# Performance work log

Measured on AMD Instinct MI355X. Metric: run time of the kernel, lower is better.

## Reference

```python
import jax, jax.numpy as jnp
import numpy as np

# Irreps config: node = 64x0e + 32x1o, edge sh = 1x0e + 1x1o
N, E = 50000, 800000
MUL0, MUL1 = 64, 32
D_IN = MUL0 + 3 * MUL1          # 160
FC_H = 64
W_NUMEL = MUL0 + MUL0 + MUL1 + MUL1  # 192, per-instruction uvu weights
SQRT3 = 1.7320508075688772
ACT_C = 1.6791   # e3nn normalize2mom constant for silu


def setup_inputs() -> dict:
    key = jax.random.key(0)
    ks = jax.random.split(key, 11)
    return {
        "x": jax.random.normal(ks[0], (N, D_IN), jnp.float32),
        "edge_scalars": jax.random.uniform(ks[1], (E, FC_H), dtype=jnp.float32),
        "edge_attr_sh": jax.random.normal(ks[2], (E, 4), jnp.float32),
        "edge_index": jax.random.randint(ks[3], (2, E), 0, N),
        "w_fc1": jax.random.normal(ks[4], (FC_H, FC_H), jnp.float32),
        "w_fc2": jax.random.normal(ks[5], (FC_H, W_NUMEL), jnp.float32),
        "w_sc_s": jax.random.normal(ks[6], (MUL0, MUL0), jnp.float32),
        "w_sc_v": jax.random.normal(ks[7], (MUL1, MUL1), jnp.float32),
        "w_lin_s": jax.random.normal(ks[8], (96, MUL0), jnp.float32),
        "w_lin_v": jax.random.normal(ks[9], (96, MUL1), jnp.float32),
        "w_alpha": jax.random.normal(ks[10], (96, 1), jnp.float32) * 0.1,
    }


def reference(x, edge_scalars, edge_attr_sh, edge_index, w_fc1, w_fc2,
              w_sc_s, w_sc_v, w_lin_s, w_lin_v, w_alpha):
    src, dst = edge_index[0], edge_index[1]

    # --- fc: FullyConnectedNet([64, 64, 192], silu), e3nn fan-in norm ---
    h = jax.nn.silu(edge_scalars @ w_fc1 / np.sqrt(FC_H)) * ACT_C
    weight = h @ w_fc2 / np.sqrt(FC_H)                       # [E, 192]
    w0 = weight[:, :MUL0]                 # 0e x 0e -> 0e (mul 64)
    w1 = weight[:, MUL0:2 * MUL0]         # 0e x 1o -> 1o (mul 64)
    w2 = weight[:, 2 * MUL0:2 * MUL0 + MUL1]   # 1o x 0e -> 1o (mul 32)
    w3 = weight[:, 2 * MUL0 + MUL1:]           # 1o x 1o -> 0e (mul 32)

    # --- self connection: o3.Linear(in -> out), per-irrep mixing ---
    x_s = x[:, :MUL0]                                   # [N, 64]
    x_v = x[:, MUL0:].reshape(N, MUL1, 3)               # [N, 32, 3]
    sc_s = x_s @ w_sc_s / np.sqrt(MUL0)
    sc_v = jnp.einsum('nui,uw->nwi', x_v, w_sc_v) / np.sqrt(MUL1)
    sc_out = jnp.concatenate([sc_s, sc_v.reshape(N, 3 * MUL1)], axis=1)

    # --- gather + edge-weighted uvu tensor product ---
    gx_s = x_s[src]                                     # [E, 64]
    gx_v = x_v[src]                                     # [E, 32, 3]
    sh_s = edge_attr_sh[:, 0:1]                         # [E, 1]
    sh_v = edge_attr_sh[:, 1:4]                         # [E, 3]

    # path weights fold with w3j so factors cancel for 1o outputs
    mid_s0 = w0 * gx_s * sh_s                                        # [E,64] 0e
    mid_s1 = w3 * jnp.einsum('eui,ei->eu', gx_v, sh_v) / SQRT3       # [E,32] 0e
    mid_v0 = w1[:, :, None] * gx_s[:, :, None] * sh_v[:, None, :]    # [E,64,3] 1o
    mid_v1 = w2[:, :, None] * gx_v * sh_s[:, :, None]                # [E,32,3] 1o
    edge_feat = jnp.concatenate(
        [mid_s0, mid_s1, mid_v0.reshape(E, 3 * MUL0), mid_v1.reshape(E, 3 * MUL1)],
        axis=1)                                                      # [E, 384]

    # --- scatter-mean to destination nodes ---
    seg = jax.ops.segment_sum(edge_feat, dst, num_segments=N)
    cnt = jax.ops.segment_sum(jnp.ones((E,), edge_feat.dtype), dst, num_segments=N)
    mean = seg / jnp.maximum(cnt, 1.0)[:, None]                      # [N, 384]

    m_s = mean[:, :96]                                   # 96x0e
    m_v = mean[:, 96:].reshape(N, 96, 3)                 # 96x1o

    # --- alpha gate (o3.Linear mid -> 0e) and output linear ---
    alpha = m_s @ w_alpha / np.sqrt(96)                  # [N, 1]
    lin_s = m_s @ w_lin_s / np.sqrt(96)                  # [N, 64]
    lin_v = jnp.einsum('nui,uw->nwi', m_v, w_lin_v) / np.sqrt(96)
    lin_out = jnp.concatenate([lin_s, lin_v.reshape(N, 3 * MUL1)], axis=1)

    # sc.output_mask is all-ones here (every output irrep reachable)
    return sc_out + alpha * lin_out
```

## Files before the change

kernel.cpp:

```cpp
#include <hip/hip_runtime.h>
#include <hip/hip_bf16.h>

#define N_NODES 50000
#define N_EDGES 800000
#define MUL0 64
#define MUL1 32
#define D_IN 160
#define FC_H 64
#define W_NUMEL 192
#define FEAT 384
#define ACT_C 1.6791f
#define INV_SQRT3 0.57735026918962576f
#define RSQRT32 0.17677669529663687f
#define RSQRT96 0.10206207261596575f

#define TILE 64
#define NWG_EDGE (N_EDGES / TILE)

typedef __attribute__((ext_vector_type(8))) short s16x8;
typedef __attribute__((ext_vector_type(4))) float f32x4;
typedef _Float16 h8 __attribute__((ext_vector_type(8)));
typedef __fp16 fp16x2 __attribute__((ext_vector_type(2)));

static __device__ __forceinline__ unsigned short f2bf(float f) {
    __hip_bfloat16 b = __float2bfloat16(f);
    return __builtin_bit_cast(unsigned short, b);
}

static __device__ __forceinline__ int swz(int row, int byte_in_row) {
    int unit = ((row & 1) << 2) | (byte_in_row >> 4);
    int su = unit ^ ((row >> 1) & 7);
    return (row >> 1) * 128 + su * 16 + (byte_in_row & 15);
}
static __device__ __forceinline__ h8 rdh8(const unsigned char* base, int row, int eb) {
    return *(const h8*)(base + swz(row, eb));
}


#define HIST_NB ((N_EDGES + 255) / 256)
#define XCONV_NB ((N_NODES * D_IN + 4095) / 4096)

__global__ __launch_bounds__(256) void hist_prep_kernel(
    const int*   __restrict__ eidx,
    int*         __restrict__ cnt,
    const float* __restrict__ w_fc1,
    const float* __restrict__ w_fc2,
    const float* __restrict__ w_sc_s,
    const float* __restrict__ w_sc_v,
    const float* __restrict__ w_lin_s,
    const float* __restrict__ w_lin_v,
    const float* __restrict__ x,
    unsigned short* __restrict__ x16,
    unsigned short* __restrict__ w1t,
    unsigned short* __restrict__ w2t,
    unsigned short* __restrict__ wscs_t,
    unsigned short* __restrict__ wscv_t,
    unsigned short* __restrict__ wlins_t,
    unsigned short* __restrict__ wlinv_t)
{
    int b = blockIdx.x;
    if (b < HIST_NB) {
        int e = b * 256 + threadIdx.x;
        if (e < N_EDGES) atomicAdd(&cnt[eidx[N_EDGES + e]], 1);
    } else if (b < HIST_NB + 48) {
        int i = (b - HIST_NB) * 256 + threadIdx.x;
        if (i < 64 * 64)  w1t[i]    = f2bf(w_fc1[(i & 63) * FC_H + (i >> 6)]);
        if (i < 192 * 64) w2t[i]    = f2bf(w_fc2[(i & 63) * W_NUMEL + (i >> 6)]);
        if (i < 64 * 64)  wscs_t[i] = f2bf(w_sc_s[(i & 63) * 64 + (i >> 6)]);
        if (i < 32 * 32)  wscv_t[i] = f2bf(w_sc_v[(i & 31) * 32 + (i >> 5)]);
        if (i < 64 * 96)  wlins_t[i] = f2bf(w_lin_s[(i % 96) * 64 + (i / 96)]);
        if (i < 32 * 96)  wlinv_t[i] = f2bf(w_lin_v[(i % 96) * 32 + (i / 96)]);
    } else {
        size_t i0 = ((size_t)(b - HIST_NB - 48) * 256 + threadIdx.x) * 16;
        if (i0 < (size_t)N_NODES * D_IN) {
            const float4* src = (const float4*)(x + i0);
            unsigned short u[16];
#pragma unroll
            for (int k = 0; k < 4; ++k) {
                float4 v = src[k];
                u[k * 4 + 0] = __builtin_bit_cast(unsigned short, (_Float16)v.x);
                u[k * 4 + 1] = __builtin_bit_cast(unsigned short, (_Float16)v.y);
                u[k * 4 + 2] = __builtin_bit_cast(unsigned short, (_Float16)v.z);
                u[k * 4 + 3] = __builtin_bit_cast(unsigned short, (_Float16)v.w);
            }
            uint4* dst = (uint4*)(x16 + i0);
            dst[0] = *(const uint4*)&u[0];
            dst[1] = *(const uint4*)&u[8];
        }
    }
}

#define SCAN_NB 64
#define SCAN_CH ((N_NODES + SCAN_NB - 1) / SCAN_NB)

__global__ __launch_bounds__(256) void scanA_kernel(const int* __restrict__ cnt,
                                                    int* __restrict__ bsum) {
    __shared__ int sred[4];
    int b = blockIdx.x, t = threadIdx.x;
    int lim = min((b + 1) * SCAN_CH, N_NODES);
    int s = 0;
    for (int i = b * SCAN_CH + t; i < lim; i += 256) s += cnt[i];
    for (int d = 1; d < 64; d <<= 1) s += __shfl_xor(s, d);
    if ((t & 63) == 0) sred[t >> 6] = s;
    __syncthreads();
    if (t == 0) bsum[b] = sred[0] + sred[1] + sred[2] + sred[3];
}

__global__ __launch_bounds__(256) void scanC_kernel(const int* __restrict__ cnt,
                                                    const int* __restrict__ bsum,
                                                    int* __restrict__ fill) {
    __shared__ int s_w[4];
    __shared__ int s_boff;
    int b = blockIdx.x, t = threadIdx.x;
    if (t < 64) {
        int v = bsum[t];
        int p = v;
        for (int d = 1; d < 64; d <<= 1) { int u = __shfl_up(p, d); if (t >= d) p += u; }
        if (t == b) s_boff = p - v;
    }
    const int CH2 = (SCAN_CH + 255) / 256;
    int base = b * SCAN_CH + t * CH2;
    int lim = min((b + 1) * SCAN_CH, N_NODES);
    int s = 0;
#pragma unroll
    for (int k = 0; k < CH2; ++k) { int i = base + k; if (i < lim) s += cnt[i]; }
    int v = s;
    for (int d = 1; d < 64; d <<= 1) { int u = __shfl_up(v, d); if ((t & 63) >= d) v += u; }
    if ((t & 63) == 63) s_w[t >> 6] = v;
    __syncthreads();
    if (t == 0) { int run = 0; for (int w = 0; w < 4; ++w) { int tv = s_w[w]; s_w[w] = run; run += tv; } }
    __syncthreads();
    int run = s_boff + s_w[t >> 6] + (v - s);
#pragma unroll
    for (int k = 0; k < CH2; ++k) {
        int i = base + k;
        if (i < lim) { fill[i] = run; run += cnt[i]; }
    }
}

__global__ __launch_bounds__(256) void scatter_ids_kernel(const int* __restrict__ eidx,
                                                          int* __restrict__ fill,
                                                          int* __restrict__ sorted_eid,
                                                          int* __restrict__ sorted_src,
                                                          int* __restrict__ sorted_dst) {
    int e = blockIdx.x * 256 + threadIdx.x;
    if (e < N_EDGES) {
        int d = eidx[N_EDGES + e];
        int s = eidx[e];
        int p = atomicAdd(&fill[d], 1);
        sorted_eid[p] = e;
        sorted_src[p] = s;
        sorted_dst[p] = d;
    }
}

#define X_OFF    0
#define W_OFF    20480
#define SH_OFF   45056
#define SID_OFF  45568
#define SEGN_OFF 45696
#define NSEG_OFF 45952
#define SMEM_SZ  45968

static __device__ __forceinline__ h8 seg_mask(const unsigned* vv, unsigned tgt) {
    h8 a;
#pragma unroll
    for (int w2 = 0; w2 < 4; ++w2) {
        a[w2 * 2]     = ((vv[w2] & 0xffffu) == tgt) ? (_Float16)1.f : (_Float16)0.f;
        a[w2 * 2 + 1] = ((vv[w2] >> 16)     == tgt) ? (_Float16)1.f : (_Float16)0.f;
    }
    return a;
}

__global__ __launch_bounds__(256) void edge_kernel(
    const unsigned short* __restrict__ x16,
    const float* __restrict__ es,
    const float* __restrict__ sh,
    const int*   __restrict__ sorted_eid,
    const int*   __restrict__ sorted_src,
    const int*   __restrict__ sorted_dst,
    const unsigned short* __restrict__ w1t,
    const unsigned short* __restrict__ w2t,
    float* __restrict__ accg)
{
    __shared__ __align__(16) unsigned char smem[SMEM_SZ];
    int* s_segnode = (int*)(smem + SEGN_OFF);
    unsigned short* s_sid = (unsigned short*)(smem + SID_OFF);

    const int t = threadIdx.x;
    const int l = t & 63;
    const int wv = t >> 6;
    const int lr = l & 15;
    const int lk = l >> 4;
    int bid;
    {
        const int nwg = NWG_EDGE;
        int orig = blockIdx.x;
        int xcd = orig & 7, idx = orig >> 3;
        int q = nwg >> 3, r = nwg & 7;
        bid = (xcd < r ? xcd * (q + 1) : r * (q + 1) + (xcd - r) * q) + idx;
    }
    const int tile0 = bid * TILE;

    int eid_own = sorted_eid[tile0 + wv * 16 + lr];
    float4 esf[4];
    {
        const float4* ep = (const float4*)(es + (size_t)eid_own * FC_H);
        esf[0] = ep[lk * 2];     esf[1] = ep[lk * 2 + 1];
        esf[2] = ep[8 + lk * 2]; esf[3] = ep[8 + lk * 2 + 1];
    }
    const int hs   = t >> 7;
    const int tt_h = t & 127;
    const int xe   = tt_h & 31;
    const int cgrp = tt_h >> 5;
    float4 xg[5];
    {
        const float4* xp = (const float4*)(x16 + (size_t)sorted_src[tile0 + hs * 32 + xe] * D_IN);
#pragma unroll
        for (int k = 0; k < 5; ++k) xg[k] = xp[cgrp * 5 + k];
    }
    float shv = sh[(size_t)sorted_eid[tile0 + (t >> 2)] * 4 + (t & 3)];
    if (wv == 0) {
        int dl = sorted_dst[tile0 + l];
        int nd = __shfl_down(dl, 1);
        bool flag = (l == 63) || (dl != nd);
        unsigned long long m = __ballot(flag);
        int sid = __popcll(m & ((1ull << l) - 1ull));
        s_sid[l] = (unsigned short)sid;
        if (flag) s_segnode[sid] = dl;
        if (l == 63) *(int*)(smem + NSEG_OFF) = sid + 1;
    }

    unsigned short* s_h = (unsigned short*)(smem + X_OFF);
    s16x8 afrag[2];
    {
        s16x8 a;
        a[0] = f2bf(esf[0].x); a[1] = f2bf(esf[0].y); a[2] = f2bf(esf[0].z); a[3] = f2bf(esf[0].w);
        a[4] = f2bf(esf[1].x); a[5] = f2bf(esf[1].y); a[6] = f2bf(esf[1].z); a[7] = f2bf(esf[1].w);
        afrag[0] = a;
        a[0] = f2bf(esf[2].x); a[1] = f2bf(esf[2].y); a[2] = f2bf(esf[2].z); a[3] = f2bf(esf[2].w);
        a[4] = f2bf(esf[3].x); a[5] = f2bf(esf[3].y); a[6] = f2bf(esf[3].z); a[7] = f2bf(esf[3].w);
        afrag[1] = a;
    }
#pragma unroll
    for (int nt = 0; nt < 4; ++nt) {
        f32x4 hacc = {0.f, 0.f, 0.f, 0.f};
#pragma unroll
        for (int kk = 0; kk < 2; ++kk) {
            s16x8 b = *(const s16x8*)(w1t + (nt * 16 + lr) * 64 + kk * 32 + lk * 8);
            hacc = __builtin_amdgcn_mfma_f32_16x16x32_bf16(afrag[kk], b, hacc, 0, 0, 0);
        }
#pragma unroll
        for (int q = 0; q < 4; ++q) {
            float aa = hacc[q] * 0.125f;
            float hv = aa * (1.f / (1.f + __expf(-aa))) * ACT_C;
            s_h[(wv * 16 + lk * 4 + q) * 72 + nt * 16 + lr] = f2bf(hv);
        }
    }
    s16x8 hfrag[2];
#pragma unroll
    for (int kk = 0; kk < 2; ++kk)
        hfrag[kk] = *(const s16x8*)(s_h + (wv * 16 + lr) * 72 + kk * 32 + lk * 8);
    __syncthreads();

    {
        const int ws = wv >> 1;
        const int ebyte = (wv & 1) * 32 + lk * 8;
        unsigned char* bw = smem + W_OFF + ws * 12288;
#pragma unroll
        for (int nt = 0; nt < 12; ++nt) {
            f32x4 acc = {0.f, 0.f, 0.f, 0.f};
#pragma unroll
            for (int kk = 0; kk < 2; ++kk) {
                s16x8 b = *(const s16x8*)(w2t + (nt * 16 + lr) * 64 + kk * 32 + lk * 8);
                acc = __builtin_amdgcn_mfma_f32_16x16x32_bf16(hfrag[kk], b, acc, 0, 0, 0);
            }
            int f = nt * 16 + lr;
            fp16x2 p0 = __builtin_amdgcn_cvt_pkrtz(acc[0] * 0.125f, acc[1] * 0.125f);
            fp16x2 p1 = __builtin_amdgcn_cvt_pkrtz(acc[2] * 0.125f, acc[3] * 0.125f);
            uint2 wval = { __builtin_bit_cast(unsigned, p0), __builtin_bit_cast(unsigned, p1) };
            *(uint2*)(bw + swz(f, ebyte)) = wval;
        }
    }
    {
        unsigned char* bx = smem + X_OFF + hs * 10240;
#pragma unroll
        for (int k = 0; k < 5; ++k) {
            unsigned short u[8];
            *(float4*)u = xg[k];
#pragma unroll
            for (int jj = 0; jj < 8; ++jj) {
                int r = (cgrp * 5 + k) * 8 + jj;
                *(unsigned short*)(bx + swz(r, xe * 2)) = u[jj];
            }
        }
    }
    {
        int e = t >> 2, c = t & 3;
        *(_Float16*)(smem + SH_OFF + (e >> 5) * 256 + swz(c, (e & 31) * 2)) = (_Float16)shv;
    }
    __syncthreads();

    const int nseg = *(const int*)(smem + NSEG_OFF);
    const int eb = lk * 16;

    h8 shreg[4][2];
    unsigned vv[2][4];
#pragma unroll
    for (int ks = 0; ks < 2; ++ks) {
#pragma unroll
        for (int r = 0; r < 4; ++r)
            shreg[r][ks] = rdh8(smem + SH_OFF + ks * 256, r, eb);
        uint4 sv = *(const uint4*)(smem + SID_OFF + ks * 64 + lk * 16);
        vv[ks][0] = sv.x; vv[ks][1] = sv.y; vv[ks][2] = sv.z; vv[ks][3] = sv.w;
    }

    h8 Bv[4][2];
    int fcol[4];
    bool cls3j[4] = {false, false, false, false};
#pragma unroll
    for (int ks = 0; ks < 2; ++ks) {
        const unsigned char* bx = smem + X_OFF + ks * 10240;
        const unsigned char* bw = smem + W_OFF + ks * 12288;
        if (wv == 0) {
#pragma unroll
            for (int jj = 0; jj < 4; ++jj) {
                int col = jj * 16 + lr;
                Bv[jj][ks] = rdh8(bw, col, eb) * rdh8(bx, col, eb);
                fcol[jj] = col;
            }
        } else if (wv == 1) {
#pragma unroll
            for (int jj = 0; jj < 4; ++jj) {
                int col = jj * 16 + lr;
                Bv[jj][ks] = rdh8(bw, 128 + col / 3, eb) * rdh8(bx, 64 + col, eb);
                fcol[jj] = 288 + col;
            }
        } else if (wv == 2) {
#pragma unroll
            for (int jj = 0; jj < 2; ++jj) {
                int col = 64 + jj * 16 + lr;
                Bv[jj][ks] = rdh8(bw, 128 + col / 3, eb) * rdh8(bx, 64 + col, eb);
                fcol[jj] = 288 + col;
            }
#pragma unroll
            for (int jj = 2; jj < 4; ++jj) {
                int col = (jj - 2) * 16 + lr;
                h8 d = rdh8(bx, 64 + 3 * col, eb)     * shreg[1][ks]
                     + rdh8(bx, 64 + 3 * col + 1, eb) * shreg[2][ks]
                     + rdh8(bx, 64 + 3 * col + 2, eb) * shreg[3][ks];
                Bv[jj][ks] = rdh8(bw, 160 + col, eb) * d;
                fcol[jj] = 64 + col;
                cls3j[jj] = true;
            }
        } else {
#pragma unroll
            for (int jj = 0; jj < 4; ++jj) {
                int col = jj * 16 + lr;
                Bv[jj][ks] = rdh8(bw, 64 + col, eb) * rdh8(bx, col, eb);
                fcol[jj] = 96 + 3 * col;
            }
        }
    }

    if (wv != 3) {
        const int npass = (nseg + 15) >> 4;
        for (int p = 0; p < npass; ++p) {
            h8 bm0 = seg_mask(vv[0], (unsigned)(p * 16 + lr));
            h8 bm1 = seg_mask(vv[1], (unsigned)(p * 16 + lr));
            h8 As0 = bm0 * shreg[0][0];
            h8 As1 = bm1 * shreg[0][1];
            const int m0 = p * 16 + lk * 4;
            float* nptr[4]; bool valid[4], atq[4];
#pragma unroll
            for (int q = 0; q < 4; ++q) {
                int sg = m0 + q;
                valid[q] = sg < nseg;
                int node = valid[q] ? s_segnode[sg] : 0;
                nptr[q] = accg + (size_t)node * FEAT;
                atq[q] = (sg == 0) || (sg == nseg - 1);
            }
#pragma unroll
            for (int jj = 0; jj < 4; ++jj) {
                f32x4 acc = {0.f, 0.f, 0.f, 0.f};
                acc = __builtin_amdgcn_mfma_f32_16x16x32_f16(cls3j[jj] ? bm0 : As0, Bv[jj][0], acc, 0, 0, 0);
                acc = __builtin_amdgcn_mfma_f32_16x16x32_f16(cls3j[jj] ? bm1 : As1, Bv[jj][1], acc, 0, 0, 0);
                const float sc = cls3j[jj] ? INV_SQRT3 : 1.f;
#pragma unroll
                for (int q = 0; q < 4; ++q) {
                    if (valid[q]) {
                        float v = acc[q] * sc;
                        float* a = nptr[q] + fcol[jj];
                        if (atq[q]) atomicAdd(a, v); else *a = v;
                    }
                }
            }
        }
    } else {
        const int npass = (3 * nseg + 15) >> 4;
        for (int p = 0; p < npass; ++p) {
            int m = p * 16 + lr;
            int sgA = m / 3, i3A = m - 3 * sgA;
            h8 mk0 = seg_mask(vv[0], (unsigned)sgA);
            h8 mk1 = seg_mask(vv[1], (unsigned)sgA);
            h8 A0 = mk0 * ((i3A == 0) ? shreg[1][0] : (i3A == 1) ? shreg[2][0] : shreg[3][0]);
            h8 A1 = mk1 * ((i3A == 0) ? shreg[1][1] : (i3A == 1) ? shreg[2][1] : shreg[3][1]);
            int m0 = p * 16 + lk * 4;
            int sgq = m0 / 3, rq = m0 - 3 * sgq;
            float* nptr[4]; int i3q[4]; bool valid[4], atq[4];
#pragma unroll
            for (int q = 0; q < 4; ++q) {
                valid[q] = sgq < nseg;
                int node = valid[q] ? s_segnode[sgq] : 0;
                nptr[q] = accg + (size_t)node * FEAT;
                i3q[q] = rq;
                atq[q] = (sgq == 0) || (sgq == nseg - 1);
                if (++rq == 3) { rq = 0; ++sgq; }
            }
#pragma unroll
            for (int jj = 0; jj < 4; ++jj) {
                f32x4 acc = {0.f, 0.f, 0.f, 0.f};
                acc = __builtin_amdgcn_mfma_f32_16x16x32_f16(A0, Bv[jj][0], acc, 0, 0, 0);
                acc = __builtin_amdgcn_mfma_f32_16x16x32_f16(A1, Bv[jj][1], acc, 0, 0, 0);
#pragma unroll
                for (int q = 0; q < 4; ++q) {
                    if (valid[q]) {
                        float* a = nptr[q] + fcol[jj] + i3q[q];
                        if (atq[q]) atomicAdd(a, acc[q]); else *a = acc[q];
                    }
                }
            }
        }
    }
}


static __device__ __forceinline__ s16x8 frag_c8(const float* p, float s) {
    float4 u = *(const float4*)p, v = *(const float4*)(p + 4);
    s16x8 a;
    a[0] = f2bf(u.x * s); a[1] = f2bf(u.y * s); a[2] = f2bf(u.z * s); a[3] = f2bf(u.w * s);
    a[4] = f2bf(v.x * s); a[5] = f2bf(v.y * s); a[6] = f2bf(v.z * s); a[7] = f2bf(v.w * s);
    return a;
}

__global__ __launch_bounds__(256) void node_kernel(
    const float* __restrict__ x,
    const float* __restrict__ accg,
    const int*   __restrict__ cnt,
    const unsigned short* __restrict__ wscs_t,
    const unsigned short* __restrict__ wscv_t,
    const unsigned short* __restrict__ wlins_t,
    const unsigned short* __restrict__ wlinv_t,
    const float* __restrict__ w_alpha,
    float* __restrict__ out)
{
    const int t = threadIdx.x;
    const int wv = t >> 6, l = t & 63;
    const int lr = l & 15, lk = l >> 4;
    const int n_base = blockIdx.x * 64 + wv * 16;
    const int nrow = n_base + lr;
    const int nclamp = min(nrow, N_NODES - 1);

    const float* mrow = accg + (size_t)nclamp * FEAT;
    const float* xrow = x + (size_t)nclamp * D_IN;
    const float rinv = 1.f / (float)max(cnt[nclamp], 1);

    s16x8 ax[2], ams[3], axv[3], amv[3][3];
#pragma unroll
    for (int kk = 0; kk < 2; ++kk) ax[kk] = frag_c8(xrow + kk * 32 + lk * 8, 1.f);
#pragma unroll
    for (int kk = 0; kk < 3; ++kk) ams[kk] = frag_c8(mrow + kk * 32 + lk * 8, rinv);
    {
        float xb[24];
        const float4* p = (const float4*)(xrow + 64 + 24 * lk);
#pragma unroll
        for (int q = 0; q < 6; ++q) ((float4*)xb)[q] = p[q];
#pragma unroll
        for (int i = 0; i < 3; ++i) {
            s16x8 a;
#pragma unroll
            for (int j = 0; j < 8; ++j) a[j] = f2bf(xb[3 * j + i]);
            axv[i] = a;
        }
    }
#pragma unroll
    for (int kk = 0; kk < 3; ++kk) {
        float mb[24];
        const float4* p = (const float4*)(mrow + 96 + 96 * kk + 24 * lk);
#pragma unroll
        for (int q = 0; q < 6; ++q) ((float4*)mb)[q] = p[q];
#pragma unroll
        for (int i = 0; i < 3; ++i) {
            s16x8 a;
#pragma unroll
            for (int j = 0; j < 8; ++j) a[j] = f2bf(mb[3 * j + i] * rinv);
            amv[i][kk] = a;
        }
    }

    float ap = 0.f;
    {
        float ab[24];
        const float4* p = (const float4*)(mrow + 24 * lk);
#pragma unroll
        for (int q = 0; q < 6; ++q) ((float4*)ab)[q] = p[q];
#pragma unroll
        for (int j = 0; j < 24; ++j) ap += ab[j] * rinv * w_alpha[lk * 24 + j];
    }
    ap += __shfl_xor(ap, 16);
    ap += __shfl_xor(ap, 32);
    const float alphav = ap * RSQRT96;

    f32x4 accA[4], accL[4];
#pragma unroll
    for (int nt = 0; nt < 4; ++nt) { accA[nt] = (f32x4){0,0,0,0}; accL[nt] = (f32x4){0,0,0,0}; }
#pragma unroll
    for (int nt = 0; nt < 4; ++nt) {
#pragma unroll
        for (int kk = 0; kk < 2; ++kk) {
            s16x8 b = *(const s16x8*)(wscs_t + (nt * 16 + lr) * 64 + kk * 32 + lk * 8);
            accA[nt] = __builtin_amdgcn_mfma_f32_16x16x32_bf16(ax[kk], b, accA[nt], 0, 0, 0);
        }
#pragma unroll
        for (int kk = 0; kk < 3; ++kk) {
            s16x8 b = *(const s16x8*)(wlins_t + (nt * 16 + lr) * 96 + kk * 32 + lk * 8);
            accL[nt] = __builtin_amdgcn_mfma_f32_16x16x32_bf16(ams[kk], b, accL[nt], 0, 0, 0);
        }
    }
    f32x4 accVs[3][2], accVl[3][2];
#pragma unroll
    for (int i = 0; i < 3; ++i)
#pragma unroll
        for (int nt = 0; nt < 2; ++nt) { accVs[i][nt] = (f32x4){0,0,0,0}; accVl[i][nt] = (f32x4){0,0,0,0}; }
#pragma unroll
    for (int i = 0; i < 3; ++i) {
#pragma unroll
        for (int nt = 0; nt < 2; ++nt) {
            s16x8 b = *(const s16x8*)(wscv_t + (nt * 16 + lr) * 32 + lk * 8);
            accVs[i][nt] = __builtin_amdgcn_mfma_f32_16x16x32_bf16(axv[i], b, accVs[i][nt], 0, 0, 0);
#pragma unroll
            for (int kk = 0; kk < 3; ++kk) {
                s16x8 b2 = *(const s16x8*)(wlinv_t + (nt * 16 + lr) * 96 + kk * 32 + lk * 8);
                accVl[i][nt] = __builtin_amdgcn_mfma_f32_16x16x32_bf16(amv[i][kk], b2, accVl[i][nt], 0, 0, 0);
            }
        }
    }

#pragma unroll
    for (int q = 0; q < 4; ++q) {
        int row = lk * 4 + q;
        float ar = __shfl(alphav, row);
        int n = n_base + row;
        bool ok = (n < N_NODES);
        float* orow = out + (size_t)n * 160;
#pragma unroll
        for (int nt = 0; nt < 4; ++nt) {
            float vout = accA[nt][q] * 0.125f + ar * accL[nt][q] * RSQRT96;
            if (ok) orow[nt * 16 + lr] = vout;
        }
#pragma unroll
        for (int i = 0; i < 3; ++i)
#pragma unroll
            for (int nt = 0; nt < 2; ++nt) {
                float vout = accVs[i][nt][q] * RSQRT32 + ar * accVl[i][nt][q] * RSQRT96;
                if (ok) orow[64 + 3 * (nt * 16 + lr) + i] = vout;
            }
    }
}


extern "C" void kernel_launch(void* const* d_in, const int* in_sizes, int n_in,
                              void* d_out, int out_size, void* d_ws, size_t ws_size,
                              hipStream_t stream) {
    const float* x        = (const float*)d_in[0];
    const float* es       = (const float*)d_in[1];
    const float* sh       = (const float*)d_in[2];
    const int*   eidx     = (const int*)d_in[3];
    const float* w_fc1    = (const float*)d_in[4];
    const float* w_fc2    = (const float*)d_in[5];
    const float* w_sc_s   = (const float*)d_in[6];
    const float* w_sc_v   = (const float*)d_in[7];
    const float* w_lin_s  = (const float*)d_in[8];
    const float* w_lin_v  = (const float*)d_in[9];
    const float* w_alpha  = (const float*)d_in[10];
    float* out = (float*)d_out;

    float* accg       = (float*)d_ws;
    int*   cnt        = (int*)(accg + (size_t)N_NODES * FEAT);
    int*   fill       = cnt + N_NODES;
    int*   sorted_eid = fill + N_NODES;
    int*   sorted_src = sorted_eid + N_EDGES;
    int*   sorted_dst = sorted_src + N_EDGES;
    unsigned short* w1t     = (unsigned short*)(sorted_dst + N_EDGES);
    unsigned short* w2t     = w1t + 64 * 64;
    unsigned short* wscs_t  = w2t + 192 * 64;
    unsigned short* wscv_t  = wscs_t + 64 * 64;
    unsigned short* wlins_t = wscv_t + 32 * 32;
    unsigned short* wlinv_t = wlins_t + 64 * 96;
    int* bsum = (int*)(wlinv_t + 32 * 96);
    size_t base_bytes = (size_t)((unsigned char*)(bsum + SCAN_NB) - (unsigned char*)d_ws);
    base_bytes = (base_bytes + 15) & ~(size_t)15;
    unsigned short* x16 = (unsigned short*)((unsigned char*)d_ws + base_bytes);

    (void)hipMemsetAsync(d_ws, 0, ((size_t)N_NODES * FEAT + N_NODES) * 4, stream);
    hipLaunchKernelGGL(hist_prep_kernel, dim3(HIST_NB + 48 + XCONV_NB), dim3(256), 0, stream,
                       eidx, cnt, w_fc1, w_fc2, w_sc_s, w_sc_v, w_lin_s, w_lin_v,
                       x, x16, w1t, w2t, wscs_t, wscv_t, wlins_t, wlinv_t);
    hipLaunchKernelGGL(scanA_kernel, dim3(SCAN_NB), dim3(256), 0, stream, cnt, bsum);
    hipLaunchKernelGGL(scanC_kernel, dim3(SCAN_NB), dim3(256), 0, stream, cnt, bsum, fill);
    hipLaunchKernelGGL(scatter_ids_kernel, dim3((N_EDGES + 255) / 256), dim3(256), 0, stream,
                       eidx, fill, sorted_eid, sorted_src, sorted_dst);
    hipLaunchKernelGGL(edge_kernel, dim3(NWG_EDGE), dim3(256), 0, stream,
                       x16, es, sh, sorted_eid, sorted_src, sorted_dst, w1t, w2t, accg);
    hipLaunchKernelGGL(node_kernel, dim3((N_NODES + 63) / 64), dim3(256), 0, stream,
                       x, accg, cnt, wscs_t, wscv_t, wlins_t, wlinv_t, w_alpha, out);
}
```

Measured before the change: 427.8 us.

## Fold accumulator zeroing into prep kernel, merge scans, presort edge SH

```diff
diff --git a/kernel.cpp b/kernel.cpp
--- a/kernel.cpp
+++ b/kernel.cpp
@@ -37,12 +37,14 @@
 }
 
 
-#define HIST_NB ((N_EDGES + 255) / 256)
+#define ZERO_NB  18750
+#define HIST_NB  ((N_EDGES + 255) / 256)
 #define XCONV_NB ((N_NODES * D_IN + 4095) / 4096)
 
 __global__ __launch_bounds__(256) void hist_prep_kernel(
     const int*   __restrict__ eidx,
     int*         __restrict__ cnt,
+    float*       __restrict__ accg,
     const float* __restrict__ w_fc1,
     const float* __restrict__ w_fc2,
     const float* __restrict__ w_sc_s,
@@ -59,11 +61,17 @@
     unsigned short* __restrict__ wlinv_t)
 {
     int b = blockIdx.x;
-    if (b < HIST_NB) {
-        int e = b * 256 + threadIdx.x;
+    if (b < ZERO_NB) {
+        size_t i = ((size_t)b * 256 + threadIdx.x) * 4;
+        if (i < (size_t)N_NODES * FEAT) {
+            float4 z = {0.f, 0.f, 0.f, 0.f};
+            *(float4*)(accg + i) = z;
+        }
+    } else if (b < ZERO_NB + HIST_NB) {
+        int e = (b - ZERO_NB) * 256 + threadIdx.x;
         if (e < N_EDGES) atomicAdd(&cnt[eidx[N_EDGES + e]], 1);
-    } else if (b < HIST_NB + 48) {
-        int i = (b - HIST_NB) * 256 + threadIdx.x;
+    } else if (b < ZERO_NB + HIST_NB + 48) {
+        int i = (b - ZERO_NB - HIST_NB) * 256 + threadIdx.x;
         if (i < 64 * 64)  w1t[i]    = f2bf(w_fc1[(i & 63) * FC_H + (i >> 6)]);
         if (i < 192 * 64) w2t[i]    = f2bf(w_fc2[(i & 63) * W_NUMEL + (i >> 6)]);
         if (i < 64 * 64)  wscs_t[i] = f2bf(w_sc_s[(i & 63) * 64 + (i >> 6)]);
@@ -71,7 +79,7 @@
         if (i < 64 * 96)  wlins_t[i] = f2bf(w_lin_s[(i % 96) * 64 + (i / 96)]);
         if (i < 32 * 96)  wlinv_t[i] = f2bf(w_lin_v[(i % 96) * 32 + (i / 96)]);
     } else {
-        size_t i0 = ((size_t)(b - HIST_NB - 48) * 256 + threadIdx.x) * 16;
+        size_t i0 = ((size_t)(b - ZERO_NB - HIST_NB - 48) * 256 + threadIdx.x) * 16;
         if (i0 < (size_t)N_NODES * D_IN) {
             const float4* src = (const float4*)(x + i0);
             unsigned short u[16];
@@ -93,30 +101,20 @@
 #define SCAN_NB 64
 #define SCAN_CH ((N_NODES + SCAN_NB - 1) / SCAN_NB)
 
-__global__ __launch_bounds__(256) void scanA_kernel(const int* __restrict__ cnt,
-                                                    int* __restrict__ bsum) {
-    __shared__ int sred[4];
-    int b = blockIdx.x, t = threadIdx.x;
-    int lim = min((b + 1) * SCAN_CH, N_NODES);
-    int s = 0;
-    for (int i = b * SCAN_CH + t; i < lim; i += 256) s += cnt[i];
-    for (int d = 1; d < 64; d <<= 1) s += __shfl_xor(s, d);
-    if ((t & 63) == 0) sred[t >> 6] = s;
-    __syncthreads();
-    if (t == 0) bsum[b] = sred[0] + sred[1] + sred[2] + sred[3];
-}
-
-__global__ __launch_bounds__(256) void scanC_kernel(const int* __restrict__ cnt,
-                                                    const int* __restrict__ bsum,
-                                                    int* __restrict__ fill) {
+__global__ __launch_bounds__(256) void scan_kernel(const int* __restrict__ cnt,
+                                                   int* __restrict__ fill) {
     __shared__ int s_w[4];
     __shared__ int s_boff;
     int b = blockIdx.x, t = threadIdx.x;
-    if (t < 64) {
-        int v = bsum[t];
-        int p = v;
-        for (int d = 1; d < 64; d <<= 1) { int u = __shfl_up(p, d); if (t >= d) p += u; }
-        if (t == b) s_boff = p - v;
+    {
+        int lim = min(b * SCAN_CH, N_NODES);
+        int s = 0;
+        for (int i = t; i < lim; i += 256) s += cnt[i];
+        for (int d = 1; d < 64; d <<= 1) s += __shfl_xor(s, d);
+        if ((t & 63) == 0) s_w[t >> 6] = s;
+        __syncthreads();
+        if (t == 0) s_boff = s_w[0] + s_w[1] + s_w[2] + s_w[3];
+        __syncthreads();
     }
     const int CH2 = (SCAN_CH + 255) / 256;
     int base = b * SCAN_CH + t * CH2;
@@ -126,11 +124,13 @@
     for (int k = 0; k < CH2; ++k) { int i = base + k; if (i < lim) s += cnt[i]; }
     int v = s;
     for (int d = 1; d < 64; d <<= 1) { int u = __shfl_up(v, d); if ((t & 63) >= d) v += u; }
+    __syncthreads();
     if ((t & 63) == 63) s_w[t >> 6] = v;
     __syncthreads();
-    if (t == 0) { int run = 0; for (int w = 0; w < 4; ++w) { int tv = s_w[w]; s_w[w] = run; run += tv; } }
-    __syncthreads();
-    int run = s_boff + s_w[t >> 6] + (v - s);
+    int woff = 0;
+#pragma unroll
+    for (int w = 0; w < 4; ++w) if (w < (t >> 6)) woff += s_w[w];
+    int run = s_boff + woff + (v - s);
 #pragma unroll
     for (int k = 0; k < CH2; ++k) {
         int i = base + k;
@@ -139,10 +139,12 @@
 }
 
 __global__ __launch_bounds__(256) void scatter_ids_kernel(const int* __restrict__ eidx,
+                                                          const float* __restrict__ sh,
                                                           int* __restrict__ fill,
                                                           int* __restrict__ sorted_eid,
                                                           int* __restrict__ sorted_src,
-                                                          int* __restrict__ sorted_dst) {
+                                                          int* __restrict__ sorted_dst,
+                                                          float* __restrict__ shs) {
     int e = blockIdx.x * 256 + threadIdx.x;
     if (e < N_EDGES) {
         int d = eidx[N_EDGES + e];
@@ -151,6 +153,7 @@
         sorted_eid[p] = e;
         sorted_src[p] = s;
         sorted_dst[p] = d;
+        *(float4*)(shs + (size_t)p * 4) = *(const float4*)(sh + (size_t)e * 4);
     }
 }
 
@@ -175,7 +178,7 @@
 __global__ __launch_bounds__(256) void edge_kernel(
     const unsigned short* __restrict__ x16,
     const float* __restrict__ es,
-    const float* __restrict__ sh,
+    const float* __restrict__ shs,
     const int*   __restrict__ sorted_eid,
     const int*   __restrict__ sorted_src,
     const int*   __restrict__ sorted_dst,
@@ -219,7 +222,7 @@
 #pragma unroll
         for (int k = 0; k < 5; ++k) xg[k] = xp[cgrp * 5 + k];
     }
-    float shv = sh[(size_t)sorted_eid[tile0 + (t >> 2)] * 4 + (t & 3)];
+    float shv = shs[(size_t)tile0 * 4 + t];
     if (wv == 0) {
         int dl = sorted_dst[tile0 + l];
         int nd = __shfl_down(dl, 1);
@@ -597,21 +600,21 @@
     unsigned short* wscv_t  = wscs_t + 64 * 64;
     unsigned short* wlins_t = wscv_t + 32 * 32;
     unsigned short* wlinv_t = wlins_t + 64 * 96;
-    int* bsum = (int*)(wlinv_t + 32 * 96);
-    size_t base_bytes = (size_t)((unsigned char*)(bsum + SCAN_NB) - (unsigned char*)d_ws);
+    int* pad = (int*)(wlinv_t + 32 * 96);
+    size_t base_bytes = (size_t)((unsigned char*)(pad + SCAN_NB) - (unsigned char*)d_ws);
     base_bytes = (base_bytes + 15) & ~(size_t)15;
     unsigned short* x16 = (unsigned short*)((unsigned char*)d_ws + base_bytes);
-
-    (void)hipMemsetAsync(d_ws, 0, ((size_t)N_NODES * FEAT + N_NODES) * 4, stream);
-    hipLaunchKernelGGL(hist_prep_kernel, dim3(HIST_NB + 48 + XCONV_NB), dim3(256), 0, stream,
-                       eidx, cnt, w_fc1, w_fc2, w_sc_s, w_sc_v, w_lin_s, w_lin_v,
+    float* shs = (float*)(x16 + (size_t)N_NODES * D_IN);
+
+    (void)hipMemsetAsync(cnt, 0, (size_t)N_NODES * 4, stream);
+    hipLaunchKernelGGL(hist_prep_kernel, dim3(ZERO_NB + HIST_NB + 48 + XCONV_NB), dim3(256), 0, stream,
+                       eidx, cnt, accg, w_fc1, w_fc2, w_sc_s, w_sc_v, w_lin_s, w_lin_v,
                        x, x16, w1t, w2t, wscs_t, wscv_t, wlins_t, wlinv_t);
-    hipLaunchKernelGGL(scanA_kernel, dim3(SCAN_NB), dim3(256), 0, stream, cnt, bsum);
-    hipLaunchKernelGGL(scanC_kernel, dim3(SCAN_NB), dim3(256), 0, stream, cnt, bsum, fill);
+    hipLaunchKernelGGL(scan_kernel, dim3(SCAN_NB), dim3(256), 0, stream, cnt, fill);
     hipLaunchKernelGGL(scatter_ids_kernel, dim3((N_EDGES + 255) / 256), dim3(256), 0, stream,
-                       eidx, fill, sorted_eid, sorted_src, sorted_dst);
+                       eidx, sh, fill, sorted_eid, sorted_src, sorted_dst, shs);
     hipLaunchKernelGGL(edge_kernel, dim3(NWG_EDGE), dim3(256), 0, stream,
-                       x16, es, sh, sorted_eid, sorted_src, sorted_dst, w1t, w2t, accg);
+                       x16, es, shs, sorted_eid, sorted_src, sorted_dst, w1t, w2t, accg);
     hipLaunchKernelGGL(node_kernel, dim3((N_NODES + 63) / 64), dim3(256), 0, stream,
                        x, accg, cnt, wscs_t, wscv_t, wlins_t, wlinv_t, w_alpha, out);
 }
```

After: 454.7 us. 1.06x slower.
